# Kernel tuning notes

Measured on AMD Instinct MI355X. Metric: run time of the kernel, lower is better.

Reference implementation:

```python
import jax, jax.numpy as jnp
import numpy as np

EPS = 1e-5

def _layernorm(h, g, b):
    mu = jnp.mean(h, axis=-1, keepdims=True)
    var = jnp.mean((h - mu) ** 2, axis=-1, keepdims=True)
    return (h - mu) / jnp.sqrt(var + EPS) * g + b

def _linoss_scan_im(A, dt, Bu):
    # A, dt: (N,) real; Bu: (B, L, N) complex64.
    # IM discretization of z' = -A x + B u, x' = z (LinOSS paper Eq. 3-4),
    # computed with a 2x2 block-diagonal associative (parallel) scan.
    S = 1.0 / (1.0 + dt * dt * A)  # Schur complement
    m11 = 1.0 - dt * dt * A * S
    m12 = -dt * A * S
    m21 = dt * S
    m22 = S
    fz = (m11 * dt) * Bu
    fx = (m21 * dt) * Bu
    Bt, L, N = Bu.shape
    br = lambda m: jnp.broadcast_to(m.astype(Bu.dtype), (Bt, L, N))
    elems = (br(m11), br(m12), br(m21), br(m22), fz, fx)

    def binop(ei, ej):
        a11i, a12i, a21i, a22i, bzi, bxi = ei
        a11j, a12j, a21j, a22j, bzj, bxj = ej
        return (a11j * a11i + a12j * a21i,
                a11j * a12i + a12j * a22i,
                a21j * a11i + a22j * a21i,
                a21j * a12i + a22j * a22i,
                a11j * bzi + a12j * bxi + bzj,
                a21j * bzi + a22j * bxi + bxj)

    res = jax.lax.associative_scan(binop, elems, axis=1)
    return res[5]  # x-component of the state, (B, L, N) complex

def setup_inputs():
    key = jax.random.key(0)
    ks = jax.random.split(key, 20)
    B, L, H_in, D_mod = 8, 2048, 128, 512
    s_in = np.float32(1.0 / np.sqrt(H_in))
    s_d = np.float32(1.0 / np.sqrt(D_mod))
    f32 = jnp.float32
    return {
        "x": jax.random.normal(ks[0], (B, L, H_in), f32),
        "W_in": jax.random.normal(ks[1], (D_mod, H_in), f32) * s_in,
        "b_in": jnp.zeros((D_mod,), f32),
        "W_enc": jax.random.normal(ks[2], (D_mod, D_mod), f32) * s_d,
        "b_enc": jnp.zeros((D_mod,), f32),
        "ln_g": jnp.ones((D_mod,), f32),
        "ln_b": jnp.zeros((D_mod,), f32),
        "A_diag": jax.random.uniform(ks[3], (D_mod,), f32),
        "log_steps": jax.random.normal(ks[4], (D_mod,), f32) * 0.5,
        "B_re": jax.random.normal(ks[5], (D_mod, D_mod), f32) * s_d,
        "B_im": jax.random.normal(ks[6], (D_mod, D_mod), f32) * s_d,
        "C_re": jax.random.normal(ks[7], (D_mod, D_mod), f32) * s_d,
        "C_im": jax.random.normal(ks[8], (D_mod, D_mod), f32) * s_d,
        "D": jax.random.normal(ks[9], (D_mod,), f32),
        "glu_w1": jax.random.normal(ks[10], (D_mod, D_mod), f32) * s_d,
        "glu_b1": jnp.zeros((D_mod,), f32),
        "glu_w2": jax.random.normal(ks[11], (D_mod, D_mod), f32) * s_d,
        "glu_b2": jnp.zeros((D_mod,), f32),
        "W_dec": jax.random.normal(ks[12], (D_mod, D_mod), f32) * s_d,
        "b_dec": jnp.zeros((D_mod,), f32),
        "W_out": jax.random.normal(ks[13], (H_in, D_mod), f32) * s_d,
        "b_out": jnp.zeros((H_in,), f32),
    }

def reference(x, W_in, b_in, W_enc, b_enc, ln_g, ln_b, A_diag, log_steps,
              B_re, B_im, C_re, C_im, D, glu_w1, glu_b1, glu_w2, glu_b2,
              W_dec, b_dec, W_out, b_out):
    h = x @ W_in.T + b_in                       # outer in_proj: (B, L, d)
    h = h @ W_enc.T + b_enc                     # LinOSS encoder
    skip = h
    hn = _layernorm(h, ln_g, ln_b)
    A = jax.nn.relu(A_diag)                     # nonnegative oscillator freqs
    dt = jax.nn.sigmoid(log_steps)              # per-state timestep in (0,1)
    Bc = (B_re + 1j * B_im).astype(jnp.complex64)
    Cc = (C_re + 1j * C_im).astype(jnp.complex64)
    Bu = jnp.einsum('blh,nh->bln', hn.astype(jnp.complex64), Bc)
    xs = _linoss_scan_im(A, dt, Bu)             # (B, L, N) complex
    y = jnp.einsum('bln,hn->blh', xs, Cc).real + D * hn
    y = jax.nn.gelu(y)
    y = (y @ glu_w1.T + glu_b1) * jax.nn.sigmoid(y @ glu_w2.T + glu_b2)  # GLU
    h = skip + y                                # residual (dropout = eval mode)
    h = h @ W_dec.T + b_dec                     # LinOSS decoder
    return h @ W_out.T + b_out                  # outer out_proj: (B, L, out)
```

## Files before the change

### kernel.cpp

```cpp
#include <hip/hip_runtime.h>
#include <cstddef>
#include <cstdint>
#include <math.h>

typedef _Float16 f16;
typedef f16 f16x8 __attribute__((ext_vector_type(8)));
typedef f16 f16x4 __attribute__((ext_vector_type(4)));
typedef float f32x4 __attribute__((ext_vector_type(4)));

constexpr int Bb   = 8;
constexpr int Ll   = 2048;
constexpr int Hin  = 128;
constexpr int Dm   = 512;
constexpr int Mrows = Bb * Ll;
constexpr int NC   = 32;
constexpr int CL   = Ll / NC;
constexpr int SZ1  = Bb * NC * Dm;
constexpr int SD   = 1024;

static __device__ __forceinline__ float sigmoid_f(float x) {
    return 1.f / (1.f + expf(-x));
}
static __device__ __forceinline__ float gelu_tanh_f(float x) {
    float x3 = x * x * x;
    float t  = tanhf(0.7978845608028654f * (x + 0.044715f * x3));
    return 0.5f * x * (1.f + t);
}

static __device__ __forceinline__ void gld16(const f16* g, f16* l) {
    __builtin_amdgcn_global_load_lds(
        (const __attribute__((address_space(1))) void*)g,
        (__attribute__((address_space(3))) void*)l, 16, 0, 0);
}

__global__ __launch_bounds__(128) void fuse_wc1(
    const float* __restrict__ Wenc, const float* __restrict__ Win,
    const float* __restrict__ b_in, const float* __restrict__ b_enc,
    f16* __restrict__ Wc1, float* __restrict__ bc1)
{
    const int d2 = blockIdx.x;
    const int t  = threadIdx.x;
    float acc = 0.f;
    for (int d = 0; d < Dm; ++d)
        acc = fmaf(Wenc[d2 * Dm + d], Win[d * Hin + t], acc);
    Wc1[d2 * Hin + t] = (f16)acc;
    if (t == 0) {
        float s = 0.f;
        for (int d = 0; d < Dm; ++d) s = fmaf(Wenc[d2 * Dm + d], b_in[d], s);
        bc1[d2] = s + b_enc[d2];
    }
}

__global__ __launch_bounds__(512) void fuse_wc2(
    const float* __restrict__ Wout, const float* __restrict__ Wdec,
    const float* __restrict__ b_dec, const float* __restrict__ b_out,
    f16* __restrict__ Wc2, float* __restrict__ bc2)
{
    const int o = blockIdx.x;
    const int t = threadIdx.x;
    float acc = 0.f;
    for (int d = 0; d < Dm; ++d)
        acc = fmaf(Wout[o * Dm + d], Wdec[d * Dm + t], acc);
    Wc2[o * Dm + t] = (f16)acc;
    if (t == 0) {
        float s = 0.f;
        for (int d = 0; d < Dm; ++d) s = fmaf(Wout[o * Dm + d], b_dec[d], s);
        bc2[o] = s + b_out[o];
    }
}

struct CvtJob { const float* s; f16* d; int n; int lgL; int pitch; int off; };
struct CvtJobs { CvtJob j[7]; };

__global__ __launch_bounds__(256) void convert_k(CvtJobs jobs) {
    const CvtJob jb = jobs.j[blockIdx.y];
    const int i = (blockIdx.x * 256 + threadIdx.x) * 4;
    if (i >= jb.n) return;
    const float4 v = *(const float4*)(jb.s + i);
    const int row = i >> jb.lgL;
    const int c   = i & ((1 << jb.lgL) - 1);
    f16x4 o;
    o.x = (f16)v.x; o.y = (f16)v.y; o.z = (f16)v.z; o.w = (f16)v.w;
    *(f16x4*)(jb.d + (size_t)row * jb.pitch + jb.off + c) = o;
}

template <int KM, int OUTF16, int BM>
__global__ __launch_bounds__(256, 2) void gemm_mfma(
    const f16* __restrict__ A, const f16* __restrict__ W,
    const float* __restrict__ bias,
    const f16* __restrict__ EX, const float* __restrict__ DV,
    const f16* __restrict__ SK,
    void* __restrict__ Cout, int M, int N, int K)
{
    constexpr int MR   = BM / 32;
    constexpr int AELE = BM * 64;
    constexpr int BELE = 128 * 64;
    constexpr int NBUF = (KM == 4) ? 1 : 2;
    __shared__ f16 smem[NBUF * (AELE + BELE)];

    const int tid = threadIdx.x;
    const int l   = tid & 63;
    const int wid = tid >> 6;
    const int wr  = wid >> 1;
    const int wc  = wid & 1;
    const int lc  = l & 15;
    const int lr  = l >> 4;
    const int row0 = blockIdx.x * BM;
    const int col0 = blockIdx.y * 128;

    const int NT = K >> 6;
    const int swz  = (l & 7) << 4;
    const int off0 = ((lr * 16) ^ swz) >> 1;
    const int off1 = ((64 + lr * 16) ^ swz) >> 1;

    f32x4 acc[MR][4];
#pragma unroll
    for (int i = 0; i < MR; ++i)
#pragma unroll
        for (int j = 0; j < 4; ++j) acc[i][j] = (f32x4){0.f, 0.f, 0.f, 0.f};

    auto stage_a = [&](f16* dst, const f16* src, int rs) {
#pragma unroll
        for (int c = 0; c < MR; ++c) {
            const int chunk = c * 256 + tid;
            const int row   = chunk >> 3;
            const int kb    = ((chunk & 7) << 4) ^ ((row & 7) << 4);
            gld16(src + (size_t)row * rs + (kb >> 1), dst + chunk * 8);
        }
    };
    auto stage_b = [&](f16* dst, const f16* src, int rs) {
#pragma unroll
        for (int c = 0; c < 4; ++c) {
            const int chunk = c * 256 + tid;
            const int row   = chunk >> 3;
            const int kb    = ((chunk & 7) << 4) ^ ((row & 7) << 4);
            gld16(src + (size_t)row * rs + (kb >> 1), dst + chunk * 8);
        }
    };
    auto compute = [&](const f16* As, const f16* Bs) {
#pragma unroll
        for (int ks = 0; ks < 2; ++ks) {
            const int off = ks ? off1 : off0;
            f16x8 aF[MR], bF[4];
#pragma unroll
            for (int mi = 0; mi < MR; ++mi)
                aF[mi] = *(const f16x8*)(As + (wr * (BM / 2) + mi * 16 + lc) * 64 + off);
#pragma unroll
            for (int ni = 0; ni < 4; ++ni)
                bF[ni] = *(const f16x8*)(Bs + (wc * 64 + ni * 16 + lc) * 64 + off);
#pragma unroll
            for (int mi = 0; mi < MR; ++mi)
#pragma unroll
                for (int ni = 0; ni < 4; ++ni)
                    acc[mi][ni] = __builtin_amdgcn_mfma_f32_16x16x32_f16(
                        aF[mi], bF[ni], acc[mi][ni], 0, 0, 0);
        }
    };

    if constexpr (KM != 4) {
        stage_a(smem, A + (size_t)row0 * K, K);
        stage_b(smem + NBUF * AELE, W + (size_t)col0 * K, K);
        int cur = 0;
        for (int kt = 0; kt < NT; ++kt) {
            if (kt + 1 < NT) {
                const int k1 = (kt + 1) << 6;
                stage_a(smem + (cur ^ 1) * AELE, A + (size_t)row0 * K + k1, K);
                stage_b(smem + NBUF * AELE + (cur ^ 1) * BELE, W + (size_t)col0 * K + k1, K);
                if constexpr (MR == 4)      asm volatile("s_waitcnt vmcnt(8)" ::: "memory");
                else if constexpr (MR == 2) asm volatile("s_waitcnt vmcnt(6)" ::: "memory");
                else                        asm volatile("s_waitcnt vmcnt(5)" ::: "memory");
            } else {
                asm volatile("s_waitcnt vmcnt(0)" ::: "memory");
            }
            __builtin_amdgcn_s_barrier();
            compute(smem + cur * AELE, smem + NBUF * AELE + cur * BELE);
            __builtin_amdgcn_s_barrier();
            cur ^= 1;
        }
    } else {
        f16* As = smem;
        f16* Bs = smem + AELE;
        for (int kt = 0; kt < NT; ++kt) {
            const int k0 = kt << 6;
            __syncthreads();
#pragma unroll
            for (int c = 0; c < MR; ++c) {
                const int chunk = c * 256 + tid;
                const int row   = chunk >> 3;
                const int ke    = ((((chunk & 7) << 4) ^ ((row & 7) << 4)) >> 1);
                const size_t pb = (size_t)(row0 + row) * SD + k0 + ke;
                const f16x8 p1 = *(const f16x8*)(A + pb);
                const f16x8 p2 = *(const f16x8*)(A + pb + 512);
                const f16x8 sv = *(const f16x8*)(SK + (size_t)(row0 + row) * 512 + k0 + ke);
                f16x8 h;
#pragma unroll
                for (int j = 0; j < 8; ++j)
                    h[j] = (f16)((float)sv[j] + (float)p1[j] * sigmoid_f((float)p2[j]));
                *(f16x8*)(As + chunk * 8) = h;
            }
            stage_b(Bs, W + (size_t)col0 * K + k0, K);
            __syncthreads();
            compute(As, Bs);
        }
    }

    float* Cf32 = (float*)Cout;
    f16*   Cf16 = (f16*)Cout;
#pragma unroll
    for (int mi = 0; mi < MR; ++mi) {
#pragma unroll
        for (int ni = 0; ni < 4; ++ni) {
            const int col   = col0 + wc * 64 + ni * 16 + lc;
            const int rbase = row0 + wr * (BM / 2) + mi * 16 + lr * 4;
            const f32x4 v = acc[mi][ni];
            if (KM == 1) {
                const float dv = DV[col];
#pragma unroll
                for (int r = 0; r < 4; ++r) {
                    const size_t idx = (size_t)(rbase + r) * N + col;
                    const float o = gelu_tanh_f(v[r] + dv * (float)EX[idx]);
                    if (OUTF16) Cf16[idx] = (f16)o; else Cf32[idx] = o;
                }
            } else {
                const float bv = bias ? bias[col] : 0.f;
#pragma unroll
                for (int r = 0; r < 4; ++r) {
                    const float o = v[r] + bv;
                    const size_t idx = (size_t)(rbase + r) * N + col;
                    if (OUTF16) Cf16[idx] = (f16)o; else Cf32[idx] = o;
                }
            }
        }
    }
}

__global__ __launch_bounds__(256) void layernorm_f16(
    const f16* __restrict__ X, const float* __restrict__ g,
    const float* __restrict__ b, f16* __restrict__ Y)
{
    const int lane = threadIdx.x & 63;
    const int w    = threadIdx.x >> 6;
    const int row  = blockIdx.x * 4 + w;
    const size_t base = (size_t)row * Dm + lane * 8;

    const f16x8 v = *(const f16x8*)(X + base);
    float x[8];
    float s = 0.f, q = 0.f;
#pragma unroll
    for (int i = 0; i < 8; ++i) {
        x[i] = (float)v[i];
        s += x[i]; q += x[i] * x[i];
    }
#pragma unroll
    for (int off = 32; off > 0; off >>= 1) {
        s += __shfl_xor(s, off);
        q += __shfl_xor(q, off);
    }
    const float mu  = s * (1.f / 512.f);
    const float var = q * (1.f / 512.f) - mu * mu;
    const float rs  = rsqrtf(var + 1e-5f);

    const float4 g0 = *(const float4*)(g + lane * 8);
    const float4 g1 = *(const float4*)(g + lane * 8 + 4);
    const float4 b0 = *(const float4*)(b + lane * 8);
    const float4 b1 = *(const float4*)(b + lane * 8 + 4);
    const float gg[8] = {g0.x, g0.y, g0.z, g0.w, g1.x, g1.y, g1.z, g1.w};
    const float bb[8] = {b0.x, b0.y, b0.z, b0.w, b1.x, b1.y, b1.z, b1.w};
    f16x8 o;
#pragma unroll
    for (int i = 0; i < 8; ++i)
        o[i] = (f16)((x[i] - mu) * rs * gg[i] + bb[i]);
    *(f16x8*)(Y + base) = o;
}

__global__ void consts_k(const float* __restrict__ A_diag,
                         const float* __restrict__ log_steps,
                         const float* __restrict__ glu_b1,
                         const float* __restrict__ glu_b2,
                         float* __restrict__ cst, float* __restrict__ BG)
{
    const int n = threadIdx.x;
    const float a   = fmaxf(A_diag[n], 0.f);
    const float dt  = 1.f / (1.f + expf(-log_steps[n]));
    const float d2a = dt * dt * a;
    const float S   = 1.f / (1.f + d2a);
    const float m11 = 1.f - d2a * S;
    const float m12 = -dt * a * S;
    const float m21 = dt * S;
    const float m22 = S;
    cst[n]            = m11;
    cst[Dm + n]       = m12;
    cst[2 * Dm + n]   = m21;
    cst[3 * Dm + n]   = m22;
    cst[4 * Dm + n]   = m11 * dt;
    cst[5 * Dm + n]   = m21 * dt;
    BG[n]       = glu_b1[n];
    BG[Dm + n]  = glu_b2[n];
}

__global__ __launch_bounds__(512) void scan_phase1(
    const f16* __restrict__ BU, const float* __restrict__ cst,
    float* __restrict__ S1)
{
    const int n = threadIdx.x;
    const int c = blockIdx.x & (NC - 1);
    const int b = blockIdx.x >> 5;
    const float m11 = cst[n],          m12 = cst[Dm + n];
    const float m21 = cst[2 * Dm + n], m22 = cst[3 * Dm + n];
    const float c1  = cst[4 * Dm + n], c2  = cst[5 * Dm + n];

    float zr = 0.f, xr = 0.f, zi = 0.f, xi = 0.f;
    const size_t base = ((size_t)b * Ll + (size_t)c * CL) * SD + n;
#pragma unroll 4
    for (int t = 0; t < CL; ++t) {
        const float br = (float)BU[base + (size_t)t * SD];
        const float bi = (float)BU[base + (size_t)t * SD + 512];
        const float zrn = fmaf(m11, zr, fmaf(m12, xr, c1 * br));
        const float xrn = fmaf(m21, zr, fmaf(m22, xr, c2 * br));
        const float zin = fmaf(m11, zi, fmaf(m12, xi, c1 * bi));
        const float xin = fmaf(m21, zi, fmaf(m22, xi, c2 * bi));
        zr = zrn; xr = xrn; zi = zin; xi = xin;
    }
    const int idx = blockIdx.x * Dm + n;
    S1[idx]            = zr;
    S1[SZ1 + idx]      = xr;
    S1[2 * SZ1 + idx]  = zi;
    S1[3 * SZ1 + idx]  = xi;
}

__global__ __launch_bounds__(256) void scan_phase2(
    const float* __restrict__ S1, const float* __restrict__ cst,
    float* __restrict__ G)
{
    const int gidx = blockIdx.x * 256 + threadIdx.x;
    const int n = gidx & (Dm - 1);
    const int b = gidx >> 9;
    const float m11 = cst[n],          m12 = cst[Dm + n];
    const float m21 = cst[2 * Dm + n], m22 = cst[3 * Dm + n];

    float p11 = 1.f, p12 = 0.f, p21 = 0.f, p22 = 1.f;
    for (int i = 0; i < CL; ++i) {
        const float q11 = m11 * p11 + m12 * p21;
        const float q12 = m11 * p12 + m12 * p22;
        const float q21 = m21 * p11 + m22 * p21;
        const float q22 = m21 * p12 + m22 * p22;
        p11 = q11; p12 = q12; p21 = q21; p22 = q22;
    }

    float gzr = 0.f, gxr = 0.f, gzi = 0.f, gxi = 0.f;
    for (int c = 0; c < NC; ++c) {
        const int idx = (b * NC + c) * Dm + n;
        G[idx]           = gzr;
        G[SZ1 + idx]     = gxr;
        G[2 * SZ1 + idx] = gzi;
        G[3 * SZ1 + idx] = gxi;
        const float szr = S1[idx],           sxr = S1[SZ1 + idx];
        const float szi = S1[2 * SZ1 + idx], sxi = S1[3 * SZ1 + idx];
        const float t1 = p11 * gzr + p12 * gxr + szr;
        const float t2 = p21 * gzr + p22 * gxr + sxr;
        const float t3 = p11 * gzi + p12 * gxi + szi;
        const float t4 = p21 * gzi + p22 * gxi + sxi;
        gzr = t1; gxr = t2; gzi = t3; gxi = t4;
    }
}

__global__ __launch_bounds__(512) void scan_phase3(
    const f16* __restrict__ BU, const float* __restrict__ cst,
    const float* __restrict__ G, f16* __restrict__ XS)
{
    const int n = threadIdx.x;
    const int c = blockIdx.x & (NC - 1);
    const int b = blockIdx.x >> 5;
    const float m11 = cst[n],          m12 = cst[Dm + n];
    const float m21 = cst[2 * Dm + n], m22 = cst[3 * Dm + n];
    const float c1  = cst[4 * Dm + n], c2  = cst[5 * Dm + n];

    const int sidx = blockIdx.x * Dm + n;
    float zr = G[sidx];
    float xr = G[SZ1 + sidx];
    float zi = G[2 * SZ1 + sidx];
    float xi = G[3 * SZ1 + sidx];

    const size_t base = ((size_t)b * Ll + (size_t)c * CL) * SD + n;
#pragma unroll 4
    for (int t = 0; t < CL; ++t) {
        const float br = (float)BU[base + (size_t)t * SD];
        const float bi = (float)BU[base + (size_t)t * SD + 512];
        const float zrn = fmaf(m11, zr, fmaf(m12, xr, c1 * br));
        const float xrn = fmaf(m21, zr, fmaf(m22, xr, c2 * br));
        const float zin = fmaf(m11, zi, fmaf(m12, xi, c1 * bi));
        const float xin = fmaf(m21, zi, fmaf(m22, xi, c2 * bi));
        zr = zrn; xr = xrn; zi = zin; xi = xin;
        XS[base + (size_t)t * SD]       = (f16)xr;
        XS[base + (size_t)t * SD + 512] = (f16)(-xi);
    }
}

extern "C" void kernel_launch(void* const* d_in, const int* in_sizes, int n_in,
                              void* d_out, int out_size, void* d_ws, size_t ws_size,
                              hipStream_t stream)
{
    const float* x         = (const float*)d_in[0];
    const float* W_in      = (const float*)d_in[1];
    const float* b_in      = (const float*)d_in[2];
    const float* W_enc     = (const float*)d_in[3];
    const float* b_enc     = (const float*)d_in[4];
    const float* ln_g      = (const float*)d_in[5];
    const float* ln_b      = (const float*)d_in[6];
    const float* A_diag    = (const float*)d_in[7];
    const float* log_steps = (const float*)d_in[8];
    const float* B_re      = (const float*)d_in[9];
    const float* B_im      = (const float*)d_in[10];
    const float* C_re      = (const float*)d_in[11];
    const float* C_im      = (const float*)d_in[12];
    const float* Dv        = (const float*)d_in[13];
    const float* glu_w1    = (const float*)d_in[14];
    const float* glu_b1    = (const float*)d_in[15];
    const float* glu_w2    = (const float*)d_in[16];
    const float* glu_b2    = (const float*)d_in[17];
    const float* W_dec     = (const float*)d_in[18];
    const float* b_dec     = (const float*)d_in[19];
    const float* W_out     = (const float*)d_in[20];
    const float* b_out     = (const float*)d_in[21];

    char* ws = (char*)d_ws;
    const size_t MB = 1 << 20;
    f16*   F2  = (f16*)(ws);
    f16*   F3  = (f16*)(ws + 16 * MB);
    f16*   XS  = (f16*)(ws + 32 * MB);
    f16*   BU  = (f16*)(ws + 64 * MB);
    f16*   Pp  = BU;
    f16*   GF  = (f16*)(ws + 96 * MB);
    f16*   XF  = (f16*)(ws + 112 * MB);
    float* S1  = (float*)(ws + 116 * MB);
    float* G   = (float*)(ws + 118 * MB);
    float* cst = (float*)(ws + 120 * MB);
    float* BG  = (float*)(ws + 120 * MB + 64 * 1024);
    float* bc1 = (float*)(ws + 120 * MB + 128 * 1024);
    float* bc2 = (float*)(ws + 120 * MB + 192 * 1024);
    f16*   WB  = (f16*)(ws + 121 * MB);
    f16*   WC  = (f16*)(ws + 122 * MB);
    f16*   WG  = (f16*)(ws + 123 * MB);
    f16*   Wc1 = (f16*)(ws + 124 * MB);
    f16*   Wc2 = (f16*)(ws + 124 * MB + 256 * 1024);

    CvtJobs jobs;
    jobs.j[0] = {x,      XF,            Mrows * Hin, 7, Hin,  0};
    jobs.j[1] = {B_re,   WB,            Dm * Dm,     9, Dm,   0};
    jobs.j[2] = {B_im,   WB + 512 * Dm, Dm * Dm,     9, Dm,   0};
    jobs.j[3] = {C_re,   WC,            Dm * Dm,     9, 1024, 0};
    jobs.j[4] = {C_im,   WC,            Dm * Dm,     9, 1024, 512};
    jobs.j[5] = {glu_w1, WG,            Dm * Dm,     9, Dm,   0};
    jobs.j[6] = {glu_w2, WG + 512 * Dm, Dm * Dm,     9, Dm,   0};

    convert_k<<<dim3((Mrows * Hin) / 1024, 7), 256, 0, stream>>>(jobs);
    fuse_wc1<<<Dm, Hin, 0, stream>>>(W_enc, W_in, b_in, b_enc, Wc1, bc1);
    fuse_wc2<<<Hin, Dm, 0, stream>>>(W_out, W_dec, b_dec, b_out, Wc2, bc2);
    consts_k<<<1, Dm, 0, stream>>>(A_diag, log_steps, glu_b1, glu_b2, cst, BG);

    dim3 blk(256);

    gemm_mfma<0, 1, 64><<<dim3(Mrows / 64, 4), blk, 0, stream>>>(
        XF, Wc1, bc1, nullptr, nullptr, nullptr, F2, Mrows, Dm, Hin);
    layernorm_f16<<<Mrows / 4, 256, 0, stream>>>(F2, ln_g, ln_b, F3);
    gemm_mfma<0, 1, 64><<<dim3(Mrows / 64, 8), blk, 0, stream>>>(
        F3, WB, nullptr, nullptr, nullptr, nullptr, BU, Mrows, 1024, Dm);
    scan_phase1<<<Bb * NC, 512, 0, stream>>>(BU, cst, S1);
    scan_phase2<<<(Bb * Dm) / 256, 256, 0, stream>>>(S1, cst, G);
    scan_phase3<<<Bb * NC, 512, 0, stream>>>(BU, cst, G, XS);
    gemm_mfma<1, 1, 64><<<dim3(Mrows / 64, 4), blk, 0, stream>>>(
        XS, WC, nullptr, F3, Dv, nullptr, GF, Mrows, Dm, 1024);
    gemm_mfma<0, 1, 64><<<dim3(Mrows / 64, 8), blk, 0, stream>>>(
        GF, WG, BG, nullptr, nullptr, nullptr, Pp, Mrows, 1024, Dm);
    gemm_mfma<4, 0, 32><<<dim3(Mrows / 32, 1), blk, 0, stream>>>(
        Pp, Wc2, bc2, nullptr, nullptr, F2, (float*)d_out, Mrows, Hin, Dm);
}
```

Baseline: 330.8 us.

## Fuse GLU gating and residual into GEMM epilogue; merge prep kernels

The GLU weight rows are interleaved in 64-row groups, so each 128-column GEMM tile holds matching value and gate halves. The epilogue computes the sigmoid gate through shared memory and adds the skip connection, writing h directly. This removes the 1024-wide intermediate write and its reread inside the final GEMM, which can now use the plain double-buffered pipeline. The four setup kernels are also merged into a single launch, trading extra epilogue shared-memory traffic and half-idle waves for fewer launches and less memory traffic.

```diff
diff --git a/kernel.cpp b/kernel.cpp
--- a/kernel.cpp
+++ b/kernel.cpp
@@ -33,55 +33,84 @@
         (__attribute__((address_space(3))) void*)l, 16, 0, 0);
 }
 
-__global__ __launch_bounds__(128) void fuse_wc1(
+struct CvtJob { const float* s; f16* d; int n; int lgL; int pitch; int off; int ilv; };
+struct CvtJobs { CvtJob j[7]; };
+
+__global__ __launch_bounds__(256) void prep_k(
+    CvtJobs jobs,
     const float* __restrict__ Wenc, const float* __restrict__ Win,
     const float* __restrict__ b_in, const float* __restrict__ b_enc,
-    f16* __restrict__ Wc1, float* __restrict__ bc1)
-{
-    const int d2 = blockIdx.x;
-    const int t  = threadIdx.x;
-    float acc = 0.f;
-    for (int d = 0; d < Dm; ++d)
-        acc = fmaf(Wenc[d2 * Dm + d], Win[d * Hin + t], acc);
-    Wc1[d2 * Hin + t] = (f16)acc;
-    if (t == 0) {
-        float s = 0.f;
-        for (int d = 0; d < Dm; ++d) s = fmaf(Wenc[d2 * Dm + d], b_in[d], s);
-        bc1[d2] = s + b_enc[d2];
-    }
-}
-
-__global__ __launch_bounds__(512) void fuse_wc2(
     const float* __restrict__ Wout, const float* __restrict__ Wdec,
     const float* __restrict__ b_dec, const float* __restrict__ b_out,
-    f16* __restrict__ Wc2, float* __restrict__ bc2)
-{
-    const int o = blockIdx.x;
-    const int t = threadIdx.x;
-    float acc = 0.f;
-    for (int d = 0; d < Dm; ++d)
-        acc = fmaf(Wout[o * Dm + d], Wdec[d * Dm + t], acc);
-    Wc2[o * Dm + t] = (f16)acc;
-    if (t == 0) {
-        float s = 0.f;
-        for (int d = 0; d < Dm; ++d) s = fmaf(Wout[o * Dm + d], b_dec[d], s);
-        bc2[o] = s + b_out[o];
-    }
-}
-
-struct CvtJob { const float* s; f16* d; int n; int lgL; int pitch; int off; };
-struct CvtJobs { CvtJob j[7]; };
-
-__global__ __launch_bounds__(256) void convert_k(CvtJobs jobs) {
-    const CvtJob jb = jobs.j[blockIdx.y];
-    const int i = (blockIdx.x * 256 + threadIdx.x) * 4;
-    if (i >= jb.n) return;
-    const float4 v = *(const float4*)(jb.s + i);
-    const int row = i >> jb.lgL;
-    const int c   = i & ((1 << jb.lgL) - 1);
-    f16x4 o;
-    o.x = (f16)v.x; o.y = (f16)v.y; o.z = (f16)v.z; o.w = (f16)v.w;
-    *(f16x4*)(jb.d + (size_t)row * jb.pitch + jb.off + c) = o;
+    const float* __restrict__ A_diag, const float* __restrict__ log_steps,
+    const float* __restrict__ gb1, const float* __restrict__ gb2,
+    f16* __restrict__ Wc1, float* __restrict__ bc1,
+    f16* __restrict__ Wc2, float* __restrict__ bc2,
+    float* __restrict__ cst, float* __restrict__ BG)
+{
+    const int y = blockIdx.y;
+    if (y < 7) {
+        const CvtJob jb = jobs.j[y];
+        const int mask = (1 << jb.lgL) - 1;
+        for (int i = (blockIdx.x * 256 + threadIdx.x) * 4; i < jb.n; i += 512 * 256 * 4) {
+            const float4 v = *(const float4*)(jb.s + i);
+            const int row = i >> jb.lgL;
+            const int c   = i & mask;
+            f16* dp = jb.ilv
+                ? jb.d + (size_t)(((row >> 6) << 7) + (row & 63) + jb.off) * jb.pitch + c
+                : jb.d + (size_t)row * jb.pitch + jb.off + c;
+            f16x4 o;
+            o.x = (f16)v.x; o.y = (f16)v.y; o.z = (f16)v.z; o.w = (f16)v.w;
+            *(f16x4*)dp = o;
+        }
+    } else if (y == 7) {
+        if (blockIdx.x >= 256) return;
+        const int d2 = blockIdx.x * 2 + (threadIdx.x >> 7);
+        const int t  = threadIdx.x & 127;
+        float acc = 0.f;
+        for (int d = 0; d < Dm; ++d)
+            acc = fmaf(Wenc[d2 * Dm + d], Win[d * Hin + t], acc);
+        Wc1[d2 * Hin + t] = (f16)acc;
+        if (t == 0) {
+            float s = 0.f;
+            for (int d = 0; d < Dm; ++d) s = fmaf(Wenc[d2 * Dm + d], b_in[d], s);
+            bc1[d2] = s + b_enc[d2];
+        }
+    } else if (y == 8) {
+        if (blockIdx.x >= 128) return;
+        const int o = blockIdx.x;
+        for (int t = threadIdx.x; t < Dm; t += 256) {
+            float acc = 0.f;
+            for (int d = 0; d < Dm; ++d)
+                acc = fmaf(Wout[o * Dm + d], Wdec[d * Dm + t], acc);
+            Wc2[o * Dm + t] = (f16)acc;
+        }
+        if (threadIdx.x == 0) {
+            float s = 0.f;
+            for (int d = 0; d < Dm; ++d) s = fmaf(Wout[o * Dm + d], b_dec[d], s);
+            bc2[o] = s + b_out[o];
+        }
+    } else {
+        const int n = blockIdx.x * 256 + threadIdx.x;
+        if (blockIdx.x >= 2 || n >= Dm) return;
+        const float a   = fmaxf(A_diag[n], 0.f);
+        const float dt  = 1.f / (1.f + expf(-log_steps[n]));
+        const float d2a = dt * dt * a;
+        const float S   = 1.f / (1.f + d2a);
+        const float m11 = 1.f - d2a * S;
+        const float m12 = -dt * a * S;
+        const float m21 = dt * S;
+        const float m22 = S;
+        cst[n]            = m11;
+        cst[Dm + n]       = m12;
+        cst[2 * Dm + n]   = m21;
+        cst[3 * Dm + n]   = m22;
+        cst[4 * Dm + n]   = m11 * dt;
+        cst[5 * Dm + n]   = m21 * dt;
+        const int j = n >> 6, loc = n & 63;
+        BG[(j << 7) + loc]      = gb1[n];
+        BG[(j << 7) + 64 + loc] = gb2[n];
+    }
 }
 
 template <int KM, int OUTF16, int BM>
@@ -89,14 +118,12 @@
     const f16* __restrict__ A, const f16* __restrict__ W,
     const float* __restrict__ bias,
     const f16* __restrict__ EX, const float* __restrict__ DV,
-    const f16* __restrict__ SK,
     void* __restrict__ Cout, int M, int N, int K)
 {
     constexpr int MR   = BM / 32;
     constexpr int AELE = BM * 64;
     constexpr int BELE = 128 * 64;
-    constexpr int NBUF = (KM == 4) ? 1 : 2;
-    __shared__ f16 smem[NBUF * (AELE + BELE)];
+    __shared__ f16 smem[2 * (AELE + BELE)];
 
     const int tid = threadIdx.x;
     const int l   = tid & 63;
@@ -157,55 +184,66 @@
         }
     };
 
-    if constexpr (KM != 4) {
-        stage_a(smem, A + (size_t)row0 * K, K);
-        stage_b(smem + NBUF * AELE, W + (size_t)col0 * K, K);
-        int cur = 0;
-        for (int kt = 0; kt < NT; ++kt) {
-            if (kt + 1 < NT) {
-                const int k1 = (kt + 1) << 6;
-                stage_a(smem + (cur ^ 1) * AELE, A + (size_t)row0 * K + k1, K);
-                stage_b(smem + NBUF * AELE + (cur ^ 1) * BELE, W + (size_t)col0 * K + k1, K);
-                if constexpr (MR == 4)      asm volatile("s_waitcnt vmcnt(8)" ::: "memory");
-                else if constexpr (MR == 2) asm volatile("s_waitcnt vmcnt(6)" ::: "memory");
-                else                        asm volatile("s_waitcnt vmcnt(5)" ::: "memory");
-            } else {
-                asm volatile("s_waitcnt vmcnt(0)" ::: "memory");
-            }
-            __builtin_amdgcn_s_barrier();
-            compute(smem + cur * AELE, smem + NBUF * AELE + cur * BELE);
-            __builtin_amdgcn_s_barrier();
-            cur ^= 1;
-        }
-    } else {
-        f16* As = smem;
-        f16* Bs = smem + AELE;
-        for (int kt = 0; kt < NT; ++kt) {
-            const int k0 = kt << 6;
-            __syncthreads();
-#pragma unroll
-            for (int c = 0; c < MR; ++c) {
-                const int chunk = c * 256 + tid;
-                const int row   = chunk >> 3;
-                const int ke    = ((((chunk & 7) << 4) ^ ((row & 7) << 4)) >> 1);
-                const size_t pb = (size_t)(row0 + row) * SD + k0 + ke;
-                const f16x8 p1 = *(const f16x8*)(A + pb);
-                const f16x8 p2 = *(const f16x8*)(A + pb + 512);
-                const f16x8 sv = *(const f16x8*)(SK + (size_t)(row0 + row) * 512 + k0 + ke);
-                f16x8 h;
-#pragma unroll
-                for (int j = 0; j < 8; ++j)
-                    h[j] = (f16)((float)sv[j] + (float)p1[j] * sigmoid_f((float)p2[j]));
-                *(f16x8*)(As + chunk * 8) = h;
-            }
-            stage_b(Bs, W + (size_t)col0 * K + k0, K);
-            __syncthreads();
-            compute(As, Bs);
-        }
+    stage_a(smem, A + (size_t)row0 * K, K);
+    stage_b(smem + 2 * AELE, W + (size_t)col0 * K, K);
+    int cur = 0;
+    for (int kt = 0; kt < NT; ++kt) {
+        if (kt + 1 < NT) {
+            const int k1 = (kt + 1) << 6;
+            stage_a(smem + (cur ^ 1) * AELE, A + (size_t)row0 * K + k1, K);
+            stage_b(smem + 2 * AELE + (cur ^ 1) * BELE, W + (size_t)col0 * K + k1, K);
+            if constexpr (MR == 2)      asm volatile("s_waitcnt vmcnt(6)" ::: "memory");
+            else if constexpr (MR == 1) asm volatile("s_waitcnt vmcnt(5)" ::: "memory");
+            else                        asm volatile("s_waitcnt vmcnt(8)" ::: "memory");
+        } else {
+            asm volatile("s_waitcnt vmcnt(0)" ::: "memory");
+        }
+        __builtin_amdgcn_s_barrier();
+        compute(smem + cur * AELE, smem + 2 * AELE + cur * BELE);
+        __builtin_amdgcn_s_barrier();
+        cur ^= 1;
     }
 
     float* Cf32 = (float*)Cout;
     f16*   Cf16 = (f16*)Cout;
+    if constexpr (KM == 5) {
+        float* sig = (float*)smem;
+        __syncthreads();
+        if (wc == 1) {
+#pragma unroll
+            for (int mi = 0; mi < MR; ++mi)
+#pragma unroll
+                for (int ni = 0; ni < 4; ++ni) {
+                    const int col = col0 + 64 + ni * 16 + lc;
+                    const int rl0 = wr * (BM / 2) + mi * 16 + lr * 4;
+                    const f32x4 v = acc[mi][ni];
+#pragma unroll
+                    for (int r = 0; r < 4; ++r)
+                        sig[(rl0 + r) * 65 + ni * 16 + lc] = sigmoid_f(v[r] + bias[col]);
+                }
+        }
+        __syncthreads();
+        if (wc == 0) {
+#pragma unroll
+            for (int mi = 0; mi < MR; ++mi)
+#pragma unroll
+                for (int ni = 0; ni < 4; ++ni) {
+                    const int cl   = ni * 16 + lc;
+                    const int col  = col0 + cl;
+                    const int hcol = blockIdx.y * 64 + cl;
+                    const int rl0  = wr * (BM / 2) + mi * 16 + lr * 4;
+                    const f32x4 v = acc[mi][ni];
+#pragma unroll
+                    for (int r = 0; r < 4; ++r) {
+                        const int row = row0 + rl0 + r;
+                        const float o = (float)EX[(size_t)row * Dm + hcol]
+                                      + (v[r] + bias[col]) * sig[(rl0 + r) * 65 + cl];
+                        Cf16[(size_t)row * Dm + hcol] = (f16)o;
+                    }
+                }
+        }
+        return;
+    }
 #pragma unroll
     for (int mi = 0; mi < MR; ++mi) {
 #pragma unroll
@@ -271,31 +309,6 @@
     for (int i = 0; i < 8; ++i)
         o[i] = (f16)((x[i] - mu) * rs * gg[i] + bb[i]);
     *(f16x8*)(Y + base) = o;
-}
-
-__global__ void consts_k(const float* __restrict__ A_diag,
-                         const float* __restrict__ log_steps,
-                         const float* __restrict__ glu_b1,
-                         const float* __restrict__ glu_b2,
-                         float* __restrict__ cst, float* __restrict__ BG)
-{
-    const int n = threadIdx.x;
-    const float a   = fmaxf(A_diag[n], 0.f);
-    const float dt  = 1.f / (1.f + expf(-log_steps[n]));
-    const float d2a = dt * dt * a;
-    const float S   = 1.f / (1.f + d2a);
-    const float m11 = 1.f - d2a * S;
-    const float m12 = -dt * a * S;
-    const float m21 = dt * S;
-    const float m22 = S;
-    cst[n]            = m11;
-    cst[Dm + n]       = m12;
-    cst[2 * Dm + n]   = m21;
-    cst[3 * Dm + n]   = m22;
-    cst[4 * Dm + n]   = m11 * dt;
-    cst[5 * Dm + n]   = m21 * dt;
-    BG[n]       = glu_b1[n];
-    BG[Dm + n]  = glu_b2[n];
 }
 
 __global__ __launch_bounds__(512) void scan_phase1(
@@ -429,7 +442,6 @@
     f16*   F3  = (f16*)(ws + 16 * MB);
     f16*   XS  = (f16*)(ws + 32 * MB);
     f16*   BU  = (f16*)(ws + 64 * MB);
-    f16*   Pp  = BU;
     f16*   GF  = (f16*)(ws + 96 * MB);
     f16*   XF  = (f16*)(ws + 112 * MB);
     float* S1  = (float*)(ws + 116 * MB);
@@ -445,33 +457,32 @@
     f16*   Wc2 = (f16*)(ws + 124 * MB + 256 * 1024);
 
     CvtJobs jobs;
-    jobs.j[0] = {x,      XF,            Mrows * Hin, 7, Hin,  0};
-    jobs.j[1] = {B_re,   WB,            Dm * Dm,     9, Dm,   0};
-    jobs.j[2] = {B_im,   WB + 512 * Dm, Dm * Dm,     9, Dm,   0};
-    jobs.j[3] = {C_re,   WC,            Dm * Dm,     9, 1024, 0};
-    jobs.j[4] = {C_im,   WC,            Dm * Dm,     9, 1024, 512};
-    jobs.j[5] = {glu_w1, WG,            Dm * Dm,     9, Dm,   0};
-    jobs.j[6] = {glu_w2, WG + 512 * Dm, Dm * Dm,     9, Dm,   0};
-
-    convert_k<<<dim3((Mrows * Hin) / 1024, 7), 256, 0, stream>>>(jobs);
-    fuse_wc1<<<Dm, Hin, 0, stream>>>(W_enc, W_in, b_in, b_enc, Wc1, bc1);
-    fuse_wc2<<<Hin, Dm, 0, stream>>>(W_out, W_dec, b_dec, b_out, Wc2, bc2);
-    consts_k<<<1, Dm, 0, stream>>>(A_diag, log_steps, glu_b1, glu_b2, cst, BG);
+    jobs.j[0] = {x,      XF,            Mrows * Hin, 7, Hin,  0,   0};
+    jobs.j[1] = {B_re,   WB,            Dm * Dm,     9, Dm,   0,   0};
+    jobs.j[2] = {B_im,   WB + 512 * Dm, Dm * Dm,     9, Dm,   0,   0};
+    jobs.j[3] = {C_re,   WC,            Dm * Dm,     9, 1024, 0,   0};
+    jobs.j[4] = {C_im,   WC,            Dm * Dm,     9, 1024, 512, 0};
+    jobs.j[5] = {glu_w1, WG,            Dm * Dm,     9, Dm,   0,   1};
+    jobs.j[6] = {glu_w2, WG,            Dm * Dm,     9, Dm,   64,  1};
+
+    prep_k<<<dim3(512, 10), 256, 0, stream>>>(
+        jobs, W_enc, W_in, b_in, b_enc, W_out, W_dec, b_dec, b_out,
+        A_diag, log_steps, glu_b1, glu_b2, Wc1, bc1, Wc2, bc2, cst, BG);
 
     dim3 blk(256);
 
     gemm_mfma<0, 1, 64><<<dim3(Mrows / 64, 4), blk, 0, stream>>>(
-        XF, Wc1, bc1, nullptr, nullptr, nullptr, F2, Mrows, Dm, Hin);
+        XF, Wc1, bc1, nullptr, nullptr, F2, Mrows, Dm, Hin);
     layernorm_f16<<<Mrows / 4, 256, 0, stream>>>(F2, ln_g, ln_b, F3);
     gemm_mfma<0, 1, 64><<<dim3(Mrows / 64, 8), blk, 0, stream>>>(
-        F3, WB, nullptr, nullptr, nullptr, nullptr, BU, Mrows, 1024, Dm);
+        F3, WB, nullptr, nullptr, nullptr, BU, Mrows, 1024, Dm);
     scan_phase1<<<Bb * NC, 512, 0, stream>>>(BU, cst, S1);
     scan_phase2<<<(Bb * Dm) / 256, 256, 0, stream>>>(S1, cst, G);
     scan_phase3<<<Bb * NC, 512, 0, stream>>>(BU, cst, G, XS);
     gemm_mfma<1, 1, 64><<<dim3(Mrows / 64, 4), blk, 0, stream>>>(
-        XS, WC, nullptr, F3, Dv, nullptr, GF, Mrows, Dm, 1024);
-    gemm_mfma<0, 1, 64><<<dim3(Mrows / 64, 8), blk, 0, stream>>>(
-        GF, WG, BG, nullptr, nullptr, nullptr, Pp, Mrows, 1024, Dm);
-    gemm_mfma<4, 0, 32><<<dim3(Mrows / 32, 1), blk, 0, stream>>>(
-        Pp, Wc2, bc2, nullptr, nullptr, F2, (float*)d_out, Mrows, Hin, Dm);
-}
+        XS, WC, nullptr, F3, Dv, GF, Mrows, Dm, 1024);
+    gemm_mfma<5, 1, 64><<<dim3(Mrows / 64, 8), blk, 0, stream>>>(
+        GF, WG, BG, F2, nullptr, F3, Mrows, 1024, Dm);
+    gemm_mfma<0, 0, 32><<<dim3(Mrows / 32, 1), blk, 0, stream>>>(
+        F3, Wc2, bc2, nullptr, nullptr, (float*)d_out, Mrows, Hin, Dm);
+}
```

Measured after the change: 315.5 us. -4.6%, faster.
